# Kernel tuning notes

Hardware: AMD Instinct MI355X
Metric: run time of the kernel (lower is better)

Reference implementation:

```python
import jax, jax.numpy as jnp
import numpy as np

TEMP = 0.05            # self.temp
NUM_INSTANCES = 16     # self.num_instances


def _l2norm(x):
    return x / jnp.linalg.norm(x, axis=-1, keepdims=True)


def setup_inputs() -> dict:
    key = jax.random.key(0)
    ks = jax.random.split(key, 6)
    B, D, N, K, NDATA = 256, 2048, 32768, 8192, 100000
    inputs = jax.random.normal(ks[0], (B, D), jnp.float32)
    # memory bank rows are kept unit-norm by the momentum update; init normalized
    features = _l2norm(jax.random.normal(ks[1], (N, D), jnp.float32))
    kmeans_centeroids = jax.random.normal(ks[2], (K, D), jnp.float32)
    targets = jax.random.randint(ks[3], (B,), 0, N)
    kmeans_pids = jax.random.randint(ks[4], (NDATA,), 0, K)
    indexes = jax.random.randint(ks[5], (B,), 0, NDATA)
    return {"inputs": inputs, "features": features,
            "kmeans_centeroids": kmeans_centeroids, "targets": targets,
            "kmeans_pids": kmeans_pids, "indexes": indexes, "neg_size": 20}


def reference(inputs, features, kmeans_centeroids, targets, kmeans_pids,
              indexes, neg_size):
    B = inputs.shape[0]
    K = kmeans_centeroids.shape[0]
    x = _l2norm(inputs)                                   # F.normalize(inputs, dim=1)
    outputs = x @ features.T                              # CM.forward: [B, N]
    finch_pos = jnp.take_along_axis(outputs, targets[:, None], axis=1)  # [B,1]
    kmeans_score = x @ kmeans_centeroids.T                # [B, K]
    batch_kmeans_pids = kmeans_pids[indexes]              # [B]
    # scatter_(-2) own kmeans cluster, then take top-neg_size negatives
    masked = jax.lax.stop_gradient(kmeans_score)          # detach().clone()
    masked = masked.at[jnp.arange(B), batch_kmeans_pids].set(-2.0)
    _, sel_ind_neg = jax.lax.top_k(masked, neg_size)      # [B, neg_size]
    kmeans_chosen_neg = jnp.take_along_axis(kmeans_score, sel_ind_neg, axis=1)
    mixed_score = jnp.concatenate([finch_pos, kmeans_chosen_neg], axis=1) / TEMP
    # confidence mask: per group of NUM_INSTANCES (first half of batch),
    # sample agrees with the group's modal kmeans pid (np.bincount().argmax())
    half = B // 2
    g = batch_kmeans_pids[:half].reshape(-1, NUM_INSTANCES)        # [G, I]
    counts = jax.nn.one_hot(g, K, dtype=jnp.int32).sum(axis=1)     # [G, K]
    mode = jnp.argmax(counts, axis=1)                              # ties -> smallest id
    mask_half = (g == mode[:, None]).reshape(-1).astype(jnp.float32)
    confidence_mask = jnp.concatenate([mask_half, mask_half])      # [B]
    # CE(mixed_score, 0) per-sample, confidence-weighted mean
    ce_neg = -jax.nn.log_softmax(mixed_score, axis=1)[:, 0]
    neg_con_loss = (confidence_mask * ce_neg).mean()
    # CE(outputs/temp, targets) mean
    logp = jax.nn.log_softmax(outputs / TEMP, axis=1)
    ce_main = -jnp.take_along_axis(logp, targets[:, None], axis=1).mean()
    return 0.2 * neg_con_loss + ce_main
```

## Files before the change

### kernel.cpp

```cpp
#include <hip/hip_runtime.h>
#include <stdint.h>

typedef __attribute__((ext_vector_type(8))) short short8;
typedef __attribute__((ext_vector_type(4))) float floatx4;

__device__ __forceinline__ unsigned short f2b(float f) {
    union { float f; uint32_t u; } v; v.f = f;
    uint32_t u = v.u;
    return (unsigned short)((u + 0x7FFFu + ((u >> 16) & 1u)) >> 16);
}

__device__ __forceinline__ uint32_t pk2(float a, float b) {
    union { float f; uint32_t u; } x, y; x.f = a; y.f = b;
    uint32_t ua = x.u + 0x8000u, ub = y.u + 0x8000u;
    return (ua >> 16) | (ub & 0xFFFF0000u);
}

__device__ __forceinline__ void async16(const void* g, void* l) {
    __builtin_amdgcn_global_load_lds(
        (const __attribute__((address_space(1))) void*)g,
        (__attribute__((address_space(3))) void*)l, 16, 0, 0);
}

__global__ void norm_kernel(const float* __restrict__ in,
                            unsigned short* __restrict__ xb, int D) {
    int b = blockIdx.x, t = threadIdx.x;
    const float* row = in + (size_t)b * D;
    float ss = 0.f;
    for (int i = t * 4; i < D; i += 1024) {
        float4 v = *(const float4*)(row + i);
        ss += v.x * v.x + v.y * v.y + v.z * v.z + v.w * v.w;
    }
    for (int off = 32; off > 0; off >>= 1) ss += __shfl_down(ss, off);
    __shared__ float wsum[4];
    __shared__ float rn_sh;
    if ((t & 63) == 0) wsum[t >> 6] = ss;
    __syncthreads();
    if (t == 0) rn_sh = rsqrtf(wsum[0] + wsum[1] + wsum[2] + wsum[3]);
    __syncthreads();
    float rn = rn_sh;
    unsigned short* orow = xb + (size_t)b * D;
    for (int i = t * 4; i < D; i += 1024) {
        float4 v = *(const float4*)(row + i);
        ushort4 o;
        o.x = f2b(v.x * rn); o.y = f2b(v.y * rn);
        o.z = f2b(v.z * rn); o.w = f2b(v.w * rn);
        *(ushort4*)(orow + i) = o;
    }
}

#define BKk 64
__global__ __launch_bounds__(256, 2)
void gemm_kernel(const unsigned short* __restrict__ xb,
                 const float* __restrict__ featB,
                 const float* __restrict__ centB,
                 const int* __restrict__ targets,
                 float* __restrict__ S, float* __restrict__ pos,
                 float* __restrict__ km,
                 int D, int K, int nbF) {
    __shared__ __align__(16) unsigned short Alds[256 * BKk];
    __shared__ __align__(16) unsigned short Blds[64 * BKk];

    const int t = threadIdx.x;
    const int w = t >> 6, l = t & 63;
    const bool isFeat = ((int)blockIdx.x < nbF);
    const int n0 = (isFeat ? (int)blockIdx.x : ((int)blockIdx.x - nbF)) * 64;
    const float* Bsrc = isFeat ? featB : centB;

    floatx4 acc[4][4];
#pragma unroll
    for (int ti = 0; ti < 4; ++ti)
#pragma unroll
        for (int tj = 0; tj < 4; ++tj)
            acc[ti][tj] = (floatx4){0.f, 0.f, 0.f, 0.f};

    const int kIters = D / BKk;
    const int brow = t >> 2, bq = t & 3;
    const float* bg0 = Bsrc + (size_t)(n0 + brow) * D + bq * 16;
    const int bc0 = ((bq * 2) ^ (brow & 7)) * 16;
    const int bc1 = ((bq * 2 + 1) ^ (brow & 7)) * 16;
    const char* xbB = (const char*)xb;

    for (int kt = 0; kt < kIters; ++kt) {
#pragma unroll
        for (int j = 0; j < 8; ++j) {
            int slin = j * 256 + t;
            int r = slin >> 3;
            int cg = (slin & 7) ^ (r & 7);
            async16(xbB + (size_t)r * (D * 2) + kt * (BKk * 2) + cg * 16,
                    (char*)Alds + slin * 16);
        }
        {
            const float* bg = bg0 + kt * BKk;
            float4 f0 = *(const float4*)(bg);
            float4 f1 = *(const float4*)(bg + 4);
            float4 f2 = *(const float4*)(bg + 8);
            float4 f3 = *(const float4*)(bg + 12);
            uint4 p0, p1;
            p0.x = pk2(f0.x, f0.y); p0.y = pk2(f0.z, f0.w);
            p0.z = pk2(f1.x, f1.y); p0.w = pk2(f1.z, f1.w);
            p1.x = pk2(f2.x, f2.y); p1.y = pk2(f2.z, f2.w);
            p1.z = pk2(f3.x, f3.y); p1.w = pk2(f3.z, f3.w);
            char* bb = (char*)Blds + brow * 128;
            *(uint4*)(bb + bc0) = p0;
            *(uint4*)(bb + bc1) = p1;
        }
        __syncthreads();

#pragma unroll
        for (int s = 0; s < 2; ++s) {
            short8 aF[4], bF[4];
#pragma unroll
            for (int ti = 0; ti < 4; ++ti) {
                int R = w * 64 + ti * 16 + (l & 15);
                int g = s * 4 + (l >> 4);
                aF[ti] = *(const short8*)((const char*)Alds +
                          R * 128 + ((g ^ (R & 7)) * 16));
            }
#pragma unroll
            for (int tj = 0; tj < 4; ++tj) {
                int Rn = tj * 16 + (l & 15);
                int g = s * 4 + (l >> 4);
                bF[tj] = *(const short8*)((const char*)Blds +
                          Rn * 128 + ((g ^ (Rn & 7)) * 16));
            }
#pragma unroll
            for (int ti = 0; ti < 4; ++ti)
#pragma unroll
                for (int tj = 0; tj < 4; ++tj)
                    acc[ti][tj] = __builtin_amdgcn_mfma_f32_16x16x32_bf16(
                        aF[ti], bF[tj], acc[ti][tj], 0, 0, 0);
        }
        __syncthreads();
    }

    if (isFeat) {
#pragma unroll
        for (int ti = 0; ti < 4; ++ti) {
#pragma unroll
            for (int r = 0; r < 4; ++r) {
                int row = w * 64 + ti * 16 + ((l >> 4) << 2) + r;
                int tr = targets[row];
                int col0 = n0 + (l & 15);
                float e = 0.f;
#pragma unroll
                for (int tj = 0; tj < 4; ++tj) {
                    float c = acc[ti][tj][r];
                    e += __expf(c * 20.0f);
                    if (tr == col0 + tj * 16) pos[row] = c;
                }
                e += __shfl_xor(e, 1); e += __shfl_xor(e, 2);
                e += __shfl_xor(e, 4); e += __shfl_xor(e, 8);
                if ((l & 15) == 0) atomicAdd(&S[row], e);
            }
        }
    } else {
#pragma unroll
        for (int ti = 0; ti < 4; ++ti) {
#pragma unroll
            for (int r = 0; r < 4; ++r) {
                int row = w * 64 + ti * 16 + ((l >> 4) << 2) + r;
                size_t base = (size_t)row * K + n0 + (l & 15);
#pragma unroll
                for (int tj = 0; tj < 4; ++tj)
                    km[base + tj * 16] = acc[ti][tj][r];
            }
        }
    }
}

__global__ __launch_bounds__(256, 4)
void topk_kernel(const float* __restrict__ kmr,
                 const int* __restrict__ pids,
                 const int* __restrict__ idxs,
                 const int* __restrict__ negsz,
                 float* __restrict__ topv, int K) {
    int b = blockIdx.x, t = threadIdx.x;
    int w = t >> 6, l = t & 63;
    const float* row = kmr + (size_t)b * K;
    float v[32];
#pragma unroll
    for (int k = 0; k < 32; ++k) v[k] = row[k * 256 + t];
    int gi = pids[idxs[b]];
    if ((gi & 255) == t) {
        int kk = gi >> 8;
#pragma unroll
        for (int k = 0; k < 32; ++k) if (k == kk) v[k] = -1e30f;
    }
    float bv = v[0]; int bk = 0;
#pragma unroll
    for (int k = 1; k < 32; ++k) if (v[k] > bv) { bv = v[k]; bk = k; }

    __shared__ float rv[4];
    __shared__ int rg[4];
    int ns = *negsz; if (ns > 32) ns = 32;
    for (int j = 0; j < ns; ++j) {
        float mv = bv; int mg = bk * 256 + t;
#pragma unroll
        for (int off = 1; off < 64; off <<= 1) {
            float ov = __shfl_xor(mv, off);
            int og = __shfl_xor(mg, off);
            if (ov > mv) { mv = ov; mg = og; }
        }
        if (l == 0) { rv[w] = mv; rg[w] = mg; }
        __syncthreads();
        float gv = rv[0]; int gg = rg[0];
#pragma unroll
        for (int ww = 1; ww < 4; ++ww)
            if (rv[ww] > gv) { gv = rv[ww]; gg = rg[ww]; }
        if (t == 0) topv[b * 32 + j] = gv;
        if ((gg & 255) == t) {
            int kk = gg >> 8;
#pragma unroll
            for (int k = 0; k < 32; ++k) if (k == kk) v[k] = -1e30f;
            bv = v[0]; bk = 0;
#pragma unroll
            for (int k = 1; k < 32; ++k) if (v[k] > bv) { bv = v[k]; bk = k; }
        }
        __syncthreads();
    }
}

__global__ void final_kernel(const float* __restrict__ S,
                             const float* __restrict__ pos,
                             const float* __restrict__ topv,
                             const int* __restrict__ pids,
                             const int* __restrict__ idxs,
                             const int* __restrict__ negsz,
                             float* __restrict__ out, int B) {
    __shared__ int pid_sh[256];
    __shared__ int mode_sh[16];
    __shared__ float red[256];
    int t = threadIdx.x;
    if (t < B) pid_sh[t] = pids[idxs[t]];
    __syncthreads();
    int half = B >> 1;
    int G = half / 16;
    if (t < G) {
        int bestPid = 0x7FFFFFFF, bestCnt = -1;
        for (int i = 0; i < 16; ++i) {
            int p = pid_sh[t * 16 + i];
            int c = 0;
            for (int j = 0; j < 16; ++j) c += (pid_sh[t * 16 + j] == p) ? 1 : 0;
            if (c > bestCnt || (c == bestCnt && p < bestPid)) { bestCnt = c; bestPid = p; }
        }
        mode_sh[t] = bestPid;
    }
    __syncthreads();
    float contrib = 0.f;
    if (t < B) {
        int hb = (t < half) ? t : t - half;
        float mask = (pid_sh[hb] == mode_sh[hb / 16]) ? 1.f : 0.f;
        int ns = *negsz; if (ns > 32) ns = 32;
        float p20 = pos[t] * 20.0f;
        float m = p20;
        for (int j = 0; j < ns; ++j) m = fmaxf(m, topv[t * 32 + j] * 20.0f);
        float se = __expf(p20 - m);
        for (int j = 0; j < ns; ++j) se += __expf(topv[t * 32 + j] * 20.0f - m);
        float ce_neg = m + logf(se) - p20;
        float ce_main = logf(S[t]) - p20;
        contrib = (0.2f * mask * ce_neg + ce_main) / (float)B;
    }
    red[t] = contrib;
    __syncthreads();
    for (int s = 128; s > 0; s >>= 1) {
        if (t < s) red[t] += red[t + s];
        __syncthreads();
    }
    if (t == 0) out[0] = red[0];
}

extern "C" void kernel_launch(void* const* d_in, const int* in_sizes, int n_in,
                              void* d_out, int out_size, void* d_ws, size_t ws_size,
                              hipStream_t stream) {
    const float* inputs   = (const float*)d_in[0];
    const float* features = (const float*)d_in[1];
    const float* cents    = (const float*)d_in[2];
    const int*   targets  = (const int*)d_in[3];
    const int*   pids     = (const int*)d_in[4];
    const int*   idxs     = (const int*)d_in[5];
    const int*   negsz    = (const int*)d_in[6];
    float* out = (float*)d_out;

    int Bb = in_sizes[3];
    int Dd = in_sizes[0] / Bb;
    int Nn = in_sizes[1] / Dd;
    int Kk = in_sizes[2] / Dd;

    char* ws = (char*)d_ws;
    unsigned short* xb = (unsigned short*)ws;
    size_t o = (size_t)Bb * Dd * 2;
    float* km   = (float*)(ws + o); o += (size_t)Bb * Kk * 4;
    float* S    = (float*)(ws + o); o += (size_t)Bb * 4;
    float* pos  = (float*)(ws + o); o += (size_t)Bb * 4;
    float* topv = (float*)(ws + o); o += (size_t)Bb * 32 * 4;

    hipMemsetAsync(S, 0, (size_t)Bb * 4, stream);
    norm_kernel<<<Bb, 256, 0, stream>>>(inputs, xb, Dd);
    int nbF = Nn / 64, nbC = Kk / 64;
    gemm_kernel<<<nbF + nbC, 256, 0, stream>>>(xb, features, cents, targets,
                                               S, pos, km, Dd, Kk, nbF);
    topk_kernel<<<Bb, 256, 0, stream>>>(km, pids, idxs, negsz, topv, Kk);
    final_kernel<<<1, 256, 0, stream>>>(S, pos, topv, pids, idxs, negsz, out, Bb);
}
```

Before: 493.9 us.

## Read A fragments from global, double-buffer B in LDS with register prefetch

The GEMM no longer stages the 256-row normalized input tile in LDS. Each wave reads its A fragments straight from global memory, relying on cache hits since the 1 MB bf16 activation matrix is shared by all blocks. B tiles are prefetched two iterations ahead into registers and converted into a double-buffered LDS tile, which halves the barrier count per k-step and lets global loads overlap MFMA work. The memset of S is folded into the norm kernel to drop a launch, and the occupancy hint of two blocks per CU is removed. The risks are higher latency on the uncached-LDS A reads and extra register pressure.

```diff
diff --git a/kernel.cpp b/kernel.cpp
--- a/kernel.cpp
+++ b/kernel.cpp
@@ -16,15 +16,11 @@
     return (ua >> 16) | (ub & 0xFFFF0000u);
 }
 
-__device__ __forceinline__ void async16(const void* g, void* l) {
-    __builtin_amdgcn_global_load_lds(
-        (const __attribute__((address_space(1))) void*)g,
-        (__attribute__((address_space(3))) void*)l, 16, 0, 0);
-}
-
 __global__ void norm_kernel(const float* __restrict__ in,
-                            unsigned short* __restrict__ xb, int D) {
+                            unsigned short* __restrict__ xb,
+                            float* __restrict__ S, int D) {
     int b = blockIdx.x, t = threadIdx.x;
+    if (t == 0) S[b] = 0.f;
     const float* row = in + (size_t)b * D;
     float ss = 0.f;
     for (int i = t * 4; i < D; i += 1024) {
@@ -49,8 +45,7 @@
     }
 }
 
-#define BKk 64
-__global__ __launch_bounds__(256, 2)
+__global__ __launch_bounds__(256)
 void gemm_kernel(const unsigned short* __restrict__ xb,
                  const float* __restrict__ featB,
                  const float* __restrict__ centB,
@@ -58,8 +53,7 @@
                  float* __restrict__ S, float* __restrict__ pos,
                  float* __restrict__ km,
                  int D, int K, int nbF) {
-    __shared__ __align__(16) unsigned short Alds[256 * BKk];
-    __shared__ __align__(16) unsigned short Blds[64 * BKk];
+    __shared__ __align__(16) unsigned short Blds[2][64 * 64];
 
     const int t = threadIdx.x;
     const int w = t >> 6, l = t & 63;
@@ -74,54 +68,49 @@
         for (int tj = 0; tj < 4; ++tj)
             acc[ti][tj] = (floatx4){0.f, 0.f, 0.f, 0.f};
 
-    const int kIters = D / BKk;
+    const int kIters = D / 64;
     const int brow = t >> 2, bq = t & 3;
     const float* bg0 = Bsrc + (size_t)(n0 + brow) * D + bq * 16;
-    const int bc0 = ((bq * 2) ^ (brow & 7)) * 16;
-    const int bc1 = ((bq * 2 + 1) ^ (brow & 7)) * 16;
+    const int bs0 = ((bq * 2) ^ (brow & 7)) * 16;
+    const int bs1 = ((bq * 2 + 1) ^ (brow & 7)) * 16;
     const char* xbB = (const char*)xb;
 
-    for (int kt = 0; kt < kIters; ++kt) {
-#pragma unroll
-        for (int j = 0; j < 8; ++j) {
-            int slin = j * 256 + t;
-            int r = slin >> 3;
-            int cg = (slin & 7) ^ (r & 7);
-            async16(xbB + (size_t)r * (D * 2) + kt * (BKk * 2) + cg * 16,
-                    (char*)Alds + slin * 16);
-        }
-        {
-            const float* bg = bg0 + kt * BKk;
-            float4 f0 = *(const float4*)(bg);
-            float4 f1 = *(const float4*)(bg + 4);
-            float4 f2 = *(const float4*)(bg + 8);
-            float4 f3 = *(const float4*)(bg + 12);
-            uint4 p0, p1;
-            p0.x = pk2(f0.x, f0.y); p0.y = pk2(f0.z, f0.w);
-            p0.z = pk2(f1.x, f1.y); p0.w = pk2(f1.z, f1.w);
-            p1.x = pk2(f2.x, f2.y); p1.y = pk2(f2.z, f2.w);
-            p1.z = pk2(f3.x, f3.y); p1.w = pk2(f3.z, f3.w);
-            char* bb = (char*)Blds + brow * 128;
-            *(uint4*)(bb + bc0) = p0;
-            *(uint4*)(bb + bc1) = p1;
-        }
-        __syncthreads();
-
-#pragma unroll
-        for (int s = 0; s < 2; ++s) {
-            short8 aF[4], bF[4];
+    float4 rA[4], rB[4];
+    auto loadB = [&](int kt, float4* r) {
+        const float* p = bg0 + kt * 64;
+        r[0] = *(const float4*)(p);
+        r[1] = *(const float4*)(p + 4);
+        r[2] = *(const float4*)(p + 8);
+        r[3] = *(const float4*)(p + 12);
+    };
+    auto cvtW = [&](const float4* r, int buf) {
+        uint4 p0, p1;
+        p0.x = pk2(r[0].x, r[0].y); p0.y = pk2(r[0].z, r[0].w);
+        p0.z = pk2(r[1].x, r[1].y); p0.w = pk2(r[1].z, r[1].w);
+        p1.x = pk2(r[2].x, r[2].y); p1.y = pk2(r[2].z, r[2].w);
+        p1.z = pk2(r[3].x, r[3].y); p1.w = pk2(r[3].z, r[3].w);
+        char* bb = (char*)&Blds[buf][0] + brow * 128;
+        *(uint4*)(bb + bs0) = p0;
+        *(uint4*)(bb + bs1) = p1;
+    };
+    auto compute = [&](int buf, int kt) {
+        short8 aF[2][4];
+#pragma unroll
+        for (int s2 = 0; s2 < 2; ++s2)
 #pragma unroll
             for (int ti = 0; ti < 4; ++ti) {
                 int R = w * 64 + ti * 16 + (l & 15);
-                int g = s * 4 + (l >> 4);
-                aF[ti] = *(const short8*)((const char*)Alds +
-                          R * 128 + ((g ^ (R & 7)) * 16));
+                aF[s2][ti] = *(const short8*)(xbB + (size_t)R * (D * 2) +
+                              kt * 128 + (s2 * 4 + (l >> 4)) * 16);
             }
+#pragma unroll
+        for (int s2 = 0; s2 < 2; ++s2) {
+            short8 bF[4];
 #pragma unroll
             for (int tj = 0; tj < 4; ++tj) {
                 int Rn = tj * 16 + (l & 15);
-                int g = s * 4 + (l >> 4);
-                bF[tj] = *(const short8*)((const char*)Blds +
+                int g = s2 * 4 + (l >> 4);
+                bF[tj] = *(const short8*)((const char*)&Blds[buf][0] +
                           Rn * 128 + ((g ^ (Rn & 7)) * 16));
             }
 #pragma unroll
@@ -129,8 +118,24 @@
 #pragma unroll
                 for (int tj = 0; tj < 4; ++tj)
                     acc[ti][tj] = __builtin_amdgcn_mfma_f32_16x16x32_bf16(
-                        aF[ti], bF[tj], acc[ti][tj], 0, 0, 0);
-        }
+                        aF[s2][ti], bF[tj], acc[ti][tj], 0, 0, 0);
+        }
+    };
+
+    loadB(0, rA);
+    loadB(1, rB);
+    cvtW(rA, 0);
+    __syncthreads();
+
+#pragma unroll 1
+    for (int kt = 0; kt < kIters; kt += 2) {
+        if (kt + 2 < kIters) loadB(kt + 2, rA);
+        cvtW(rB, 1);
+        compute(0, kt);
+        __syncthreads();
+        if (kt + 3 < kIters) loadB(kt + 3, rB);
+        if (kt + 2 < kIters) cvtW(rA, 0);
+        compute(1, kt + 1);
         __syncthreads();
     }
 
@@ -295,8 +300,7 @@
     float* pos  = (float*)(ws + o); o += (size_t)Bb * 4;
     float* topv = (float*)(ws + o); o += (size_t)Bb * 32 * 4;
 
-    hipMemsetAsync(S, 0, (size_t)Bb * 4, stream);
-    norm_kernel<<<Bb, 256, 0, stream>>>(inputs, xb, Dd);
+    norm_kernel<<<Bb, 256, 0, stream>>>(inputs, xb, S, Dd);
     int nbF = Nn / 64, nbC = Kk / 64;
     gemm_kernel<<<nbF + nbC, 256, 0, stream>>>(xb, features, cents, targets,
                                                S, pos, km, Dd, Kk, nbF);
```

Result: slower. 617.9 us (+25.1%).

## Double-buffer GEMM with async fp32 B loads and narrower N tiles

Applied to the files above, without the earlier changes.

Restructures the fused GEMM so both A (bf16 x) and B (fp32 features/centroids) are staged into LDS with async global-to-LDS loads into double buffers. The next k-tile is prefetched while the current one is computed, and the fp32-to-bf16 conversion of B moves to after the LDS read. The N tile shrinks from 64 to 32 and the K step from 64 to 32, which doubles the block count and raises the occupancy hint to 4. The S buffer is now zeroed inside the norm kernel, dropping the separate memset launch. In exchange, the 256-row A tile is reloaded by twice as many blocks, and the smaller tiles give fewer MFMAs per barrier.

```diff
diff --git a/kernel.cpp b/kernel.cpp
--- a/kernel.cpp
+++ b/kernel.cpp
@@ -23,8 +23,10 @@
 }
 
 __global__ void norm_kernel(const float* __restrict__ in,
-                            unsigned short* __restrict__ xb, int D) {
+                            unsigned short* __restrict__ xb,
+                            float* __restrict__ S, int D) {
     int b = blockIdx.x, t = threadIdx.x;
+    if (t == 0) S[b] = 0.f;
     const float* row = in + (size_t)b * D;
     float ss = 0.f;
     for (int i = t * 4; i < D; i += 1024) {
@@ -49,8 +51,8 @@
     }
 }
 
-#define BKk 64
-__global__ __launch_bounds__(256, 2)
+#define BKT 32
+__global__ __launch_bounds__(256, 4)
 void gemm_kernel(const unsigned short* __restrict__ xb,
                  const float* __restrict__ featB,
                  const float* __restrict__ centB,
@@ -58,80 +60,82 @@
                  float* __restrict__ S, float* __restrict__ pos,
                  float* __restrict__ km,
                  int D, int K, int nbF) {
-    __shared__ __align__(16) unsigned short Alds[256 * BKk];
-    __shared__ __align__(16) unsigned short Blds[64 * BKk];
+    __shared__ __align__(16) unsigned short Alds[2][256 * BKT];
+    __shared__ __align__(16) float Blds[2][32 * BKT];
 
     const int t = threadIdx.x;
     const int w = t >> 6, l = t & 63;
+    const int l15 = l & 15, g = l >> 4;
     const bool isFeat = ((int)blockIdx.x < nbF);
-    const int n0 = (isFeat ? (int)blockIdx.x : ((int)blockIdx.x - nbF)) * 64;
+    const int n0 = (isFeat ? (int)blockIdx.x : ((int)blockIdx.x - nbF)) * 32;
     const float* Bsrc = isFeat ? featB : centB;
-
-    floatx4 acc[4][4];
+    const char* xbB = (const char*)xb;
+    const char* BsB = (const char*)Bsrc;
+
+    floatx4 acc[4][2];
 #pragma unroll
     for (int ti = 0; ti < 4; ++ti)
 #pragma unroll
-        for (int tj = 0; tj < 4; ++tj)
+        for (int tj = 0; tj < 2; ++tj)
             acc[ti][tj] = (floatx4){0.f, 0.f, 0.f, 0.f};
 
-    const int kIters = D / BKk;
-    const int brow = t >> 2, bq = t & 3;
-    const float* bg0 = Bsrc + (size_t)(n0 + brow) * D + bq * 16;
-    const int bc0 = ((bq * 2) ^ (brow & 7)) * 16;
-    const int bc1 = ((bq * 2 + 1) ^ (brow & 7)) * 16;
-    const char* xbB = (const char*)xb;
-
+    const int kIters = D / BKT;
+
+    const int ar = t >> 2;
+    const int acg = (t & 3) ^ ((ar >> 1) & 3);
+    const int br = t >> 3;
+    const int bcg = (t & 7) ^ (br & 7);
+    const size_t bRowByte = (size_t)(n0 + br) * (D * 4) + bcg * 16;
+
+    auto stage = [&](int kt, int buf) {
+#pragma unroll
+        for (int j = 0; j < 4; ++j) {
+            int slin = j * 256 + t;
+            int r = (j * 64) + ar;
+            int cg = (t & 3) ^ ((r >> 1) & 3);
+            async16(xbB + (size_t)r * (D * 2) + kt * 64 + cg * 16,
+                    (char*)&Alds[buf][0] + slin * 16);
+        }
+        async16(BsB + bRowByte + kt * 128,
+                (char*)&Blds[buf][0] + t * 16);
+    };
+
+    auto compute = [&](int buf) {
+        short8 aF[4];
+#pragma unroll
+        for (int ti = 0; ti < 4; ++ti) {
+            int R = w * 64 + ti * 16 + l15;
+            aF[ti] = *(const short8*)((const char*)&Alds[buf][0] +
+                      R * 64 + ((g ^ ((R >> 1) & 3)) * 16));
+        }
+        short8 bF[2];
+#pragma unroll
+        for (int tj = 0; tj < 2; ++tj) {
+            int Rn = tj * 16 + l15;
+            const char* bb = (const char*)&Blds[buf][0] + Rn * 128;
+            float4 f0 = *(const float4*)(bb + (((2 * g) ^ (Rn & 7)) * 16));
+            float4 f1 = *(const float4*)(bb + (((2 * g + 1) ^ (Rn & 7)) * 16));
+            union { uint4 u; short8 s; } cv;
+            cv.u.x = pk2(f0.x, f0.y); cv.u.y = pk2(f0.z, f0.w);
+            cv.u.z = pk2(f1.x, f1.y); cv.u.w = pk2(f1.z, f1.w);
+            bF[tj] = cv.s;
+        }
+#pragma unroll
+        for (int ti = 0; ti < 4; ++ti)
+#pragma unroll
+            for (int tj = 0; tj < 2; ++tj)
+                acc[ti][tj] = __builtin_amdgcn_mfma_f32_16x16x32_bf16(
+                    aF[ti], bF[tj], acc[ti][tj], 0, 0, 0);
+    };
+
+    stage(0, 0);
+    __syncthreads();
+#pragma unroll 1
     for (int kt = 0; kt < kIters; ++kt) {
-#pragma unroll
-        for (int j = 0; j < 8; ++j) {
-            int slin = j * 256 + t;
-            int r = slin >> 3;
-            int cg = (slin & 7) ^ (r & 7);
-            async16(xbB + (size_t)r * (D * 2) + kt * (BKk * 2) + cg * 16,
-                    (char*)Alds + slin * 16);
-        }
-        {
-            const float* bg = bg0 + kt * BKk;
-            float4 f0 = *(const float4*)(bg);
-            float4 f1 = *(const float4*)(bg + 4);
-            float4 f2 = *(const float4*)(bg + 8);
-            float4 f3 = *(const float4*)(bg + 12);
-            uint4 p0, p1;
-            p0.x = pk2(f0.x, f0.y); p0.y = pk2(f0.z, f0.w);
-            p0.z = pk2(f1.x, f1.y); p0.w = pk2(f1.z, f1.w);
-            p1.x = pk2(f2.x, f2.y); p1.y = pk2(f2.z, f2.w);
-            p1.z = pk2(f3.x, f3.y); p1.w = pk2(f3.z, f3.w);
-            char* bb = (char*)Blds + brow * 128;
-            *(uint4*)(bb + bc0) = p0;
-            *(uint4*)(bb + bc1) = p1;
-        }
+        int p = kt & 1;
+        if (kt + 1 < kIters) stage(kt + 1, p ^ 1);
+        compute(p);
         __syncthreads();
-
-#pragma unroll
-        for (int s = 0; s < 2; ++s) {
-            short8 aF[4], bF[4];
-#pragma unroll
-            for (int ti = 0; ti < 4; ++ti) {
-                int R = w * 64 + ti * 16 + (l & 15);
-                int g = s * 4 + (l >> 4);
-                aF[ti] = *(const short8*)((const char*)Alds +
-                          R * 128 + ((g ^ (R & 7)) * 16));
-            }
-#pragma unroll
-            for (int tj = 0; tj < 4; ++tj) {
-                int Rn = tj * 16 + (l & 15);
-                int g = s * 4 + (l >> 4);
-                bF[tj] = *(const short8*)((const char*)Blds +
-                          Rn * 128 + ((g ^ (Rn & 7)) * 16));
-            }
-#pragma unroll
-            for (int ti = 0; ti < 4; ++ti)
-#pragma unroll
-                for (int tj = 0; tj < 4; ++tj)
-                    acc[ti][tj] = __builtin_amdgcn_mfma_f32_16x16x32_bf16(
-                        aF[ti], bF[tj], acc[ti][tj], 0, 0, 0);
-        }
-        __syncthreads();
     }
 
     if (isFeat) {
@@ -139,19 +143,19 @@
         for (int ti = 0; ti < 4; ++ti) {
 #pragma unroll
             for (int r = 0; r < 4; ++r) {
-                int row = w * 64 + ti * 16 + ((l >> 4) << 2) + r;
+                int row = w * 64 + ti * 16 + (g << 2) + r;
                 int tr = targets[row];
-                int col0 = n0 + (l & 15);
+                int col0 = n0 + l15;
                 float e = 0.f;
 #pragma unroll
-                for (int tj = 0; tj < 4; ++tj) {
+                for (int tj = 0; tj < 2; ++tj) {
                     float c = acc[ti][tj][r];
                     e += __expf(c * 20.0f);
                     if (tr == col0 + tj * 16) pos[row] = c;
                 }
                 e += __shfl_xor(e, 1); e += __shfl_xor(e, 2);
                 e += __shfl_xor(e, 4); e += __shfl_xor(e, 8);
-                if ((l & 15) == 0) atomicAdd(&S[row], e);
+                if (l15 == 0) atomicAdd(&S[row], e);
             }
         }
     } else {
@@ -159,10 +163,10 @@
         for (int ti = 0; ti < 4; ++ti) {
 #pragma unroll
             for (int r = 0; r < 4; ++r) {
-                int row = w * 64 + ti * 16 + ((l >> 4) << 2) + r;
-                size_t base = (size_t)row * K + n0 + (l & 15);
-#pragma unroll
-                for (int tj = 0; tj < 4; ++tj)
+                int row = w * 64 + ti * 16 + (g << 2) + r;
+                size_t base = (size_t)row * K + n0 + l15;
+#pragma unroll
+                for (int tj = 0; tj < 2; ++tj)
                     km[base + tj * 16] = acc[ti][tj][r];
             }
         }
@@ -295,9 +299,8 @@
     float* pos  = (float*)(ws + o); o += (size_t)Bb * 4;
     float* topv = (float*)(ws + o); o += (size_t)Bb * 32 * 4;
 
-    hipMemsetAsync(S, 0, (size_t)Bb * 4, stream);
-    norm_kernel<<<Bb, 256, 0, stream>>>(inputs, xb, Dd);
-    int nbF = Nn / 64, nbC = Kk / 64;
+    norm_kernel<<<Bb, 256, 0, stream>>>(inputs, xb, S, Dd);
+    int nbF = Nn / 32, nbC = Kk / 32;
     gemm_kernel<<<nbF + nbC, 256, 0, stream>>>(xb, features, cents, targets,
                                                S, pos, km, Dd, Kk, nbF);
     topk_kernel<<<Bb, 256, 0, stream>>>(km, pids, idxs, negsz, topv, Kk);
```

After: 611.1 us. 1.24x slower.
